# Kernel optimization log

Hardware: AMD Instinct MI355X
Metric: run time of the kernel (lower is better)

The kernel has to match this reference:

```python
import jax, jax.numpy as jnp
import numpy as np

IN_F = 1024   # in_features
OUT_F = 1024  # out_features
N = 32768     # flattened batch (prod of x.shape[:-1]))
K = 3         # clones per rewire -> denom = K + 1


def setup_inputs() -> dict:
    key = jax.random.key(0)
    k1, k2, k3, k4 = jax.random.split(key, 4)
    bound = 1.0 / np.sqrt(IN_F)
    x = jax.random.normal(k1, (N, IN_F), dtype=jnp.float32)
    # kaiming-uniform-ish init scale for weight, uniform(-bound,bound) for bias
    weight = jax.random.uniform(k2, (OUT_F, IN_F), dtype=jnp.float32,
                                minval=-bound, maxval=bound) * np.sqrt(3.0)
    bias = jax.random.uniform(k3, (OUT_F,), dtype=jnp.float32,
                              minval=-bound, maxval=bound)
    # one rewire per output row; clones are distinct from src (dead-neuron slots)
    rewire_rows = jnp.arange(OUT_F, dtype=jnp.int32)
    rewire_src = jax.random.randint(k4, (OUT_F,), 0, IN_F, dtype=jnp.int32)
    rewire_clones = (rewire_src[:, None] + jnp.arange(1, K + 1, dtype=jnp.int32)) % IN_F
    return {"x": x, "weight": weight, "bias": bias,
            "rewire_rows": rewire_rows, "rewire_src": rewire_src,
            "rewire_clones": rewire_clones}


def reference(x, weight, bias, rewire_rows, rewire_src, rewire_clones):
    # Plain linear part, shared by all output rows: y = x @ W^T + b
    base = x @ weight.T + bias                                  # [N, OUT_F]

    # Per-rewire correction. For rewire e on row r with src s and clones d_k
    # (denom = K+1), the torch loop replaces x[:, s] -> x[:, s]/denom and
    # x[:, d_k] -> x[:, s]/denom before the GEMV with weight[r].
    # Equivalent delta added to base[:, r] (indices within a rewire are disjoint):
    denom = rewire_clones.shape[1] + 1                          # K + 1
    xs = x[:, rewire_src]                                       # [N, R]
    new_val = xs / denom                                        # [N, R]
    w_src = weight[rewire_rows, rewire_src]                     # [R]
    delta = (new_val - xs) * w_src                              # src column change
    xc = x[:, rewire_clones]                                    # [N, R, K]
    wc = weight[rewire_rows[:, None], rewire_clones]            # [R, K]
    delta = delta + jnp.einsum('nrk,rk->nr', new_val[:, :, None] - xc, wc)

    # Scatter-add the deltas into their output rows (duplicates accumulate).
    return base.at[:, rewire_rows].add(delta)                   # [N, OUT_F]
```

## Files before the change

### kernel.cpp

```cpp
#include <hip/hip_runtime.h>

#define IN_F 1024
#define OUT_F 1024
#define NTOK 32768
#define BM 256
#define BN 256
#define BK 64
#define KT (IN_F / BK)

typedef __bf16 bf16;
typedef __bf16 bf16x4 __attribute__((ext_vector_type(4)));
typedef __bf16 bf16x8 __attribute__((ext_vector_type(8)));
typedef float f32x4 __attribute__((ext_vector_type(4)));

__global__ void build_wp(const float* __restrict__ W,
                         const int* __restrict__ rows,
                         const int* __restrict__ srcs,
                         const int* __restrict__ clones,
                         bf16* __restrict__ Wp) {
  const int r = blockIdx.x;
  const int row = rows[r];
  const int s = srcs[r];
  const int c0 = clones[3 * r + 0];
  const int c1 = clones[3 * r + 1];
  const int c2 = clones[3 * r + 2];
  const float* wr = W + (size_t)row * IN_F;
  const float fixv = 0.25f * (wr[s] + wr[c0] + wr[c1] + wr[c2]);

  const int col = threadIdx.x * 4;
  f32x4 v = *reinterpret_cast<const f32x4*>(wr + col);
  bf16x4 o;
#pragma unroll
  for (int j = 0; j < 4; ++j) {
    const int c = col + j;
    float f = v[j];
    if (c == c0 || c == c1 || c == c2) f = 0.0f;
    if (c == s) f = fixv;
    o[j] = (bf16)f;
  }
  *reinterpret_cast<bf16x4*>(Wp + (size_t)row * IN_F + col) = o;
}

__global__ void prep_xb(const float* __restrict__ X, bf16* __restrict__ Xb) {
  const int c = blockIdx.x * 256 + threadIdx.x;
  const int q = c & 2047;
  const int bmt = c >> 11;
  const int bm = bmt >> 4;
  const int t = bmt & 15;
  const int row = q >> 3;
  const int p = q & 7;
  const int s = p ^ (row & 7);
  const float* src = X + ((size_t)bm * BM + row) * IN_F + t * BK + s * 8;
  const f32x4 a = *reinterpret_cast<const f32x4*>(src);
  const f32x4 b = *reinterpret_cast<const f32x4*>(src + 4);
  bf16x8 o;
#pragma unroll
  for (int j = 0; j < 4; ++j) {
    o[j] = (bf16)a[j];
    o[4 + j] = (bf16)b[j];
  }
  *reinterpret_cast<bf16x8*>(Xb + (size_t)c * 8) = o;
}

__global__ __launch_bounds__(512, 2) void gemm_bf(
    const bf16* __restrict__ Xb, const bf16* __restrict__ Wp,
    const float* __restrict__ bias, float* __restrict__ out) {
  extern __shared__ __align__(16) char smem[];

  const int tid = threadIdx.x;
  const int lane = tid & 63;
  const int w = tid >> 6;
  const int wrow = w >> 2;
  const int wcol = w & 3;

  const int bid = blockIdx.x;
  const int sq = bid >> 3;
  const int bm = (bid & 7) + 8 * (sq >> 2);
  const int bn = sq & 3;

  const bf16* gA = Xb + (size_t)bm * (KT * 16384) + lane * 8;

  const bf16* gB = Wp + ((size_t)bn * BN + w * 8 + (lane >> 3)) * IN_F +
                   (((lane & 7) ^ ((lane >> 3) & 7)) * 8);

  f32x4 acc[8][4];
#pragma unroll
  for (int n = 0; n < 4; ++n) {
    const float bv = bias[bn * BN + wcol * 64 + n * 16 + (lane & 15)];
#pragma unroll
    for (int m = 0; m < 8; ++m) acc[m][n] = (f32x4){bv, bv, bv, bv};
  }

  const int rl = lane & 15;
  const int rx = rl & 7;
  const int arow0 = wrow * 128 + rl;
  const int brow0 = wcol * 64 + rl;
  const int sl0 = lane >> 4;

  auto issueA = [&](int t, int buf) {
    const bf16* g = gA + (size_t)t * 16384;
#pragma unroll
    for (int i = 0; i < 4; ++i) {
      const int chunk = i * 8 + w;
      __builtin_amdgcn_global_load_lds(
          (const __attribute__((address_space(1))) void*)(g + chunk * 512),
          (__attribute__((address_space(3))) void*)(smem + buf * 32768 +
                                                    chunk * 1024),
          16, 0, 0);
    }
  };
  auto issueB = [&](int t, int buf) {
    const bf16* g = gB + (size_t)t * BK;
    char* dst0 = smem + 65536 + buf * 32768 + w * 1024;
#pragma unroll
    for (int i = 0; i < 4; ++i) {
      __builtin_amdgcn_global_load_lds(
          (const __attribute__((address_space(1))) void*)(g +
                                                          (size_t)i * 64 * IN_F),
          (__attribute__((address_space(3))) void*)(dst0 + i * 8192), 16, 0, 0);
    }
  };
  auto compute = [&](int buf) {
    const char* A = smem + buf * 32768;
    const char* B = smem + 65536 + buf * 32768;
#pragma unroll
    for (int kk = 0; kk < 2; ++kk) {
      const int so = (((kk * 4 + sl0) ^ rx) << 4);
      bf16x8 af[8], bfr[4];
#pragma unroll
      for (int m = 0; m < 8; ++m)
        af[m] =
            *reinterpret_cast<const bf16x8*>(A + (arow0 + m * 16) * 128 + so);
#pragma unroll
      for (int n = 0; n < 4; ++n)
        bfr[n] =
            *reinterpret_cast<const bf16x8*>(B + (brow0 + n * 16) * 128 + so);
      __builtin_amdgcn_s_setprio(1);
#pragma unroll
      for (int m = 0; m < 8; ++m)
#pragma unroll
        for (int n = 0; n < 4; ++n)
          acc[m][n] = __builtin_amdgcn_mfma_f32_16x16x32_bf16(
              af[m], bfr[n], acc[m][n], 0, 0, 0);
      __builtin_amdgcn_s_setprio(0);
    }
  };

  issueA(0, 0);
  issueB(0, 0);
  __syncthreads();

  for (int t = 0; t < KT; ++t) {
    const int db = t & 1;
    if (t + 1 < KT) {
      issueA(t + 1, db ^ 1);
      issueB(t + 1, db ^ 1);
      __builtin_amdgcn_sched_barrier(0);
    }
    compute(db);
    __syncthreads();
  }

  const int orow0 = bm * BM + wrow * 128 + (lane >> 4) * 4;
  const int ocol = bn * BN + wcol * 64 + (lane & 15);
#pragma unroll
  for (int m = 0; m < 8; ++m) {
#pragma unroll
    for (int n = 0; n < 4; ++n) {
      const f32x4 v = acc[m][n];
      const size_t base = (size_t)(orow0 + m * 16) * OUT_F + (ocol + n * 16);
#pragma unroll
      for (int i = 0; i < 4; ++i) out[base + (size_t)i * OUT_F] = v[i];
    }
  }
}

__global__ __launch_bounds__(512, 2) void gemm_r4(
    const float* __restrict__ X, const bf16* __restrict__ Wp,
    const float* __restrict__ bias, float* __restrict__ out) {
  extern __shared__ __align__(16) char smem[];

  const int tid = threadIdx.x;
  const int lane = tid & 63;
  const int w = tid >> 6;
  const int wrow = w >> 2;
  const int wcol = w & 3;

  const int bid = blockIdx.x;
  const int sq = bid >> 3;
  const int bm = (bid & 7) + 8 * (sq >> 2);
  const int bn = sq & 3;

  const float* gA = X + ((size_t)bm * BM + (tid >> 3)) * IN_F + (tid & 7) * 8;
  const int awbyte =
      ((tid >> 3) << 7) + ((((tid & 7) ^ ((tid >> 3) & 7))) << 4);

  const bf16* gB = Wp + ((size_t)bn * BN + w * 8 + (lane >> 3)) * IN_F +
                   (((lane & 7) ^ ((lane >> 3) & 7)) * 8);

  f32x4 acc[8][4];
#pragma unroll
  for (int n = 0; n < 4; ++n) {
    const float bv = bias[bn * BN + wcol * 64 + n * 16 + (lane & 15)];
#pragma unroll
    for (int m = 0; m < 8; ++m) acc[m][n] = (f32x4){bv, bv, bv, bv};
  }

  const int rl = lane & 15;
  const int rx = rl & 7;
  const int arow0 = wrow * 128 + rl;
  const int brow0 = wcol * 64 + rl;
  const int sl0 = lane >> 4;

  f32x4 av[8];

  auto issueA = [&](int t) {
#pragma unroll
    for (int j = 0; j < 4; ++j) {
      const float* p = gA + (size_t)j * 64 * IN_F + (size_t)t * BK;
      av[2 * j] = *reinterpret_cast<const f32x4*>(p);
      av[2 * j + 1] = *reinterpret_cast<const f32x4*>(p + 4);
    }
  };
  auto writeA = [&](int buf) {
    char* base = smem + buf * 32768;
#pragma unroll
    for (int j = 0; j < 4; ++j) {
      bf16x8 o;
#pragma unroll
      for (int q = 0; q < 4; ++q) {
        o[q] = (bf16)av[2 * j][q];
        o[4 + q] = (bf16)av[2 * j + 1][q];
      }
      *reinterpret_cast<bf16x8*>(base + j * 8192 + awbyte) = o;
    }
  };
  auto issueB = [&](int t, int buf) {
    const bf16* g = gB + (size_t)t * BK;
    char* dst0 = smem + 65536 + buf * 32768 + w * 1024;
#pragma unroll
    for (int i = 0; i < 4; ++i) {
      __builtin_amdgcn_global_load_lds(
          (const __attribute__((address_space(1))) void*)(g +
                                                          (size_t)i * 64 * IN_F),
          (__attribute__((address_space(3))) void*)(dst0 + i * 8192), 16, 0, 0);
    }
  };
  auto compute = [&](int buf) {
    const char* A = smem + buf * 32768;
    const char* B = smem + 65536 + buf * 32768;
#pragma unroll
    for (int kk = 0; kk < 2; ++kk) {
      const int so = (((kk * 4 + sl0) ^ rx) << 4);
      bf16x8 af[8], bfr[4];
#pragma unroll
      for (int m = 0; m < 8; ++m)
        af[m] =
            *reinterpret_cast<const bf16x8*>(A + (arow0 + m * 16) * 128 + so);
#pragma unroll
      for (int n = 0; n < 4; ++n)
        bfr[n] =
            *reinterpret_cast<const bf16x8*>(B + (brow0 + n * 16) * 128 + so);
      __builtin_amdgcn_s_setprio(1);
#pragma unroll
      for (int m = 0; m < 8; ++m)
#pragma unroll
        for (int n = 0; n < 4; ++n)
          acc[m][n] = __builtin_amdgcn_mfma_f32_16x16x32_bf16(
              af[m], bfr[n], acc[m][n], 0, 0, 0);
      __builtin_amdgcn_s_setprio(0);
    }
  };

  issueA(0);
  issueB(0, 0);
  writeA(0);
  __syncthreads();

  for (int t = 0; t < KT; ++t) {
    const int db = t & 1;
    const bool more = (t + 1) < KT;
    if (more) {
      issueA(t + 1);
      issueB(t + 1, db ^ 1);
      __builtin_amdgcn_sched_barrier(0);
    }
    compute(db);
    if (more) {
      __builtin_amdgcn_sched_barrier(0);
      writeA(db ^ 1);
      __syncthreads();
    }
  }

  const int orow0 = bm * BM + wrow * 128 + (lane >> 4) * 4;
  const int ocol = bn * BN + wcol * 64 + (lane & 15);
#pragma unroll
  for (int m = 0; m < 8; ++m) {
#pragma unroll
    for (int n = 0; n < 4; ++n) {
      const f32x4 v = acc[m][n];
      const size_t base = (size_t)(orow0 + m * 16) * OUT_F + (ocol + n * 16);
#pragma unroll
      for (int i = 0; i < 4; ++i) out[base + (size_t)i * OUT_F] = v[i];
    }
  }
}

extern "C" void kernel_launch(void* const* d_in, const int* in_sizes, int n_in,
                              void* d_out, int out_size, void* d_ws,
                              size_t ws_size, hipStream_t stream) {
  const float* x = (const float*)d_in[0];
  const float* weight = (const float*)d_in[1];
  const float* bias = (const float*)d_in[2];
  const int* rrows = (const int*)d_in[3];
  const int* rsrc = (const int*)d_in[4];
  const int* rclones = (const int*)d_in[5];
  float* out = (float*)d_out;

  bf16* Wp = (bf16*)d_ws;
  bf16* Xb = (bf16*)((char*)d_ws + (2u << 20));
  const size_t need = (2u << 20) + (size_t)NTOK * IN_F * 2;

  (void)hipFuncSetAttribute((const void*)gemm_bf,
                            hipFuncAttributeMaxDynamicSharedMemorySize, 131072);
  (void)hipFuncSetAttribute((const void*)gemm_r4,
                            hipFuncAttributeMaxDynamicSharedMemorySize, 131072);

  build_wp<<<dim3(OUT_F), dim3(256), 0, stream>>>(weight, rrows, rsrc, rclones,
                                                  Wp);
  if (ws_size >= need) {
    prep_xb<<<dim3((NTOK / BM) * KT * 2048 / 256), dim3(256), 0, stream>>>(x,
                                                                           Xb);
    gemm_bf<<<dim3((NTOK / BM) * (OUT_F / BN)), dim3(512), 131072, stream>>>(
        Xb, Wp, bias, out);
  } else {
    gemm_r4<<<dim3((NTOK / BM) * (OUT_F / BN)), dim3(512), 131072, stream>>>(
        x, Wp, bias, out);
  }
}
```

Before: 116.6 us.

## Triple-buffer A tiles and prefetch two stages ahead in bf16 GEMM

The bf16 GEMM moves from a double-buffered LDS pipeline with a full __syncthreads per K-step to a three-slot ring for A tiles (two slots for B). A is prefetched two steps ahead and B one step ahead. The block barrier now waits only on partial vmcnt counts, so more global-to-LDS traffic stays in flight during MFMA compute. This raises LDS use to 160 KB and lowers launch bounds to one block per CU, giving up the second resident block in exchange for deeper prefetch. It also leans on hand-counted vmcnt values being correct.

```diff
diff --git a/kernel.cpp b/kernel.cpp
--- a/kernel.cpp
+++ b/kernel.cpp
@@ -62,7 +62,7 @@
   *reinterpret_cast<bf16x8*>(Xb + (size_t)c * 8) = o;
 }
 
-__global__ __launch_bounds__(512, 2) void gemm_bf(
+__global__ __launch_bounds__(512, 1) void gemm_bf(
     const bf16* __restrict__ Xb, const bf16* __restrict__ Wp,
     const float* __restrict__ bias, float* __restrict__ out) {
   extern __shared__ __align__(16) char smem[];
@@ -97,21 +97,21 @@
   const int brow0 = wcol * 64 + rl;
   const int sl0 = lane >> 4;
 
-  auto issueA = [&](int t, int buf) {
+  auto issueA = [&](int t, int slot) {
     const bf16* g = gA + (size_t)t * 16384;
 #pragma unroll
     for (int i = 0; i < 4; ++i) {
       const int chunk = i * 8 + w;
       __builtin_amdgcn_global_load_lds(
           (const __attribute__((address_space(1))) void*)(g + chunk * 512),
-          (__attribute__((address_space(3))) void*)(smem + buf * 32768 +
+          (__attribute__((address_space(3))) void*)(smem + slot * 32768 +
                                                     chunk * 1024),
           16, 0, 0);
     }
   };
-  auto issueB = [&](int t, int buf) {
+  auto issueB = [&](int t, int slot) {
     const bf16* g = gB + (size_t)t * BK;
-    char* dst0 = smem + 65536 + buf * 32768 + w * 1024;
+    char* dst0 = smem + 98304 + slot * 32768 + w * 1024;
 #pragma unroll
     for (int i = 0; i < 4; ++i) {
       __builtin_amdgcn_global_load_lds(
@@ -120,9 +120,9 @@
           (__attribute__((address_space(3))) void*)(dst0 + i * 8192), 16, 0, 0);
     }
   };
-  auto compute = [&](int buf) {
-    const char* A = smem + buf * 32768;
-    const char* B = smem + 65536 + buf * 32768;
+  auto compute = [&](int t) {
+    const char* A = smem + (t % 3) * 32768;
+    const char* B = smem + 98304 + (t & 1) * 32768;
 #pragma unroll
     for (int kk = 0; kk < 2; ++kk) {
       const int so = (((kk * 4 + sl0) ^ rx) << 4);
@@ -146,19 +146,26 @@
     }
   };
 
+  issueB(0, 0);
   issueA(0, 0);
-  issueB(0, 0);
-  __syncthreads();
+  issueA(1, 1);
+  asm volatile("s_waitcnt vmcnt(4)" ::: "memory");
+  __builtin_amdgcn_s_barrier();
+  __builtin_amdgcn_sched_barrier(0);
 
   for (int t = 0; t < KT; ++t) {
-    const int db = t & 1;
+    if (t + 1 < KT) issueB(t + 1, (t + 1) & 1);
+    if (t + 2 < KT) issueA(t + 2, (t + 2) % 3);
+    __builtin_amdgcn_sched_barrier(0);
+    compute(t);
     if (t + 1 < KT) {
-      issueA(t + 1, db ^ 1);
-      issueB(t + 1, db ^ 1);
+      if (t + 2 < KT)
+        asm volatile("s_waitcnt vmcnt(4)" ::: "memory");
+      else
+        asm volatile("s_waitcnt vmcnt(0)" ::: "memory");
+      __builtin_amdgcn_s_barrier();
       __builtin_amdgcn_sched_barrier(0);
     }
-    compute(db);
-    __syncthreads();
   }
 
   const int orow0 = bm * BM + wrow * 128 + (lane >> 4) * 4;
@@ -323,7 +330,7 @@
   const size_t need = (2u << 20) + (size_t)NTOK * IN_F * 2;
 
   (void)hipFuncSetAttribute((const void*)gemm_bf,
-                            hipFuncAttributeMaxDynamicSharedMemorySize, 131072);
+                            hipFuncAttributeMaxDynamicSharedMemorySize, 163840);
   (void)hipFuncSetAttribute((const void*)gemm_r4,
                             hipFuncAttributeMaxDynamicSharedMemorySize, 131072);
 
@@ -332,7 +339,7 @@
   if (ws_size >= need) {
     prep_xb<<<dim3((NTOK / BM) * KT * 2048 / 256), dim3(256), 0, stream>>>(x,
                                                                            Xb);
-    gemm_bf<<<dim3((NTOK / BM) * (OUT_F / BN)), dim3(512), 131072, stream>>>(
+    gemm_bf<<<dim3((NTOK / BM) * (OUT_F / BN)), dim3(512), 163840, stream>>>(
         Xb, Wp, bias, out);
   } else {
     gemm_r4<<<dim3((NTOK / BM) * (OUT_F / BN)), dim3(512), 131072, stream>>>(
```

Result: no change. 116.9 us (+0.3%).

## Interleave LDS reads, global prefetch and MFMA in four phases per K-tile

Applied to the files above, without the earlier changes.

Restructures the bf16 GEMM main loop into four phases per K tile. Each phase reads a slice of A fragments (B fragments are read once per tile), issues one quarter of the next tile's global-to-LDS loads, and runs 16 MFMAs. Waits and barriers are explicit (s_waitcnt and s_barrier), so memory traffic is spread across the compute instead of issued as one burst. Launch bounds are reduced to one block per SIMD group, which gives more registers but lowers occupancy. The extra barriers per tile add synchronization cost.

```diff
diff --git a/kernel.cpp b/kernel.cpp
--- a/kernel.cpp
+++ b/kernel.cpp
@@ -62,7 +62,7 @@
   *reinterpret_cast<bf16x8*>(Xb + (size_t)c * 8) = o;
 }
 
-__global__ __launch_bounds__(512, 2) void gemm_bf(
+__global__ __launch_bounds__(512, 1) void gemm_bf(
     const bf16* __restrict__ Xb, const bf16* __restrict__ Wp,
     const float* __restrict__ bias, float* __restrict__ out) {
   extern __shared__ __align__(16) char smem[];
@@ -97,68 +97,85 @@
   const int brow0 = wcol * 64 + rl;
   const int sl0 = lane >> 4;
 
-  auto issueA = [&](int t, int buf) {
+  auto gloadA1 = [&](int t, int buf, int i) {
     const bf16* g = gA + (size_t)t * 16384;
-#pragma unroll
-    for (int i = 0; i < 4; ++i) {
-      const int chunk = i * 8 + w;
-      __builtin_amdgcn_global_load_lds(
-          (const __attribute__((address_space(1))) void*)(g + chunk * 512),
-          (__attribute__((address_space(3))) void*)(smem + buf * 32768 +
-                                                    chunk * 1024),
-          16, 0, 0);
-    }
-  };
-  auto issueB = [&](int t, int buf) {
-    const bf16* g = gB + (size_t)t * BK;
-    char* dst0 = smem + 65536 + buf * 32768 + w * 1024;
-#pragma unroll
-    for (int i = 0; i < 4; ++i) {
-      __builtin_amdgcn_global_load_lds(
-          (const __attribute__((address_space(1))) void*)(g +
-                                                          (size_t)i * 64 * IN_F),
-          (__attribute__((address_space(3))) void*)(dst0 + i * 8192), 16, 0, 0);
-    }
-  };
-  auto compute = [&](int buf) {
+    const int chunk = i * 8 + w;
+    __builtin_amdgcn_global_load_lds(
+        (const __attribute__((address_space(1))) void*)(g + chunk * 512),
+        (__attribute__((address_space(3))) void*)(smem + buf * 32768 +
+                                                  chunk * 1024),
+        16, 0, 0);
+  };
+  auto gloadB1 = [&](int t, int buf, int i) {
+    const bf16* g = gB + (size_t)t * BK + (size_t)i * 64 * IN_F;
+    __builtin_amdgcn_global_load_lds(
+        (const __attribute__((address_space(1))) void*)g,
+        (__attribute__((address_space(3))) void*)(smem + 65536 + buf * 32768 +
+                                                  w * 1024 + i * 8192),
+        16, 0, 0);
+  };
+
+  bf16x8 bfr[4][2];
+  auto readB = [&](int buf) {
+    const char* B = smem + 65536 + buf * 32768;
+#pragma unroll
+    for (int n = 0; n < 4; ++n)
+#pragma unroll
+      for (int kk = 0; kk < 2; ++kk)
+        bfr[n][kk] = *reinterpret_cast<const bf16x8*>(
+            B + (brow0 + n * 16) * 128 + (((kk * 4 + sl0) ^ rx) << 4));
+  };
+  auto readA2 = [&](int buf, int m2, bf16x8 (&af)[2][2]) {
     const char* A = smem + buf * 32768;
-    const char* B = smem + 65536 + buf * 32768;
-#pragma unroll
-    for (int kk = 0; kk < 2; ++kk) {
-      const int so = (((kk * 4 + sl0) ^ rx) << 4);
-      bf16x8 af[8], bfr[4];
-#pragma unroll
-      for (int m = 0; m < 8; ++m)
-        af[m] =
-            *reinterpret_cast<const bf16x8*>(A + (arow0 + m * 16) * 128 + so);
+#pragma unroll
+    for (int dm = 0; dm < 2; ++dm)
+#pragma unroll
+      for (int kk = 0; kk < 2; ++kk)
+        af[dm][kk] = *reinterpret_cast<const bf16x8*>(
+            A + (arow0 + (m2 + dm) * 16) * 128 + (((kk * 4 + sl0) ^ rx) << 4));
+  };
+  auto mfma16 = [&](const bf16x8 (&af)[2][2], int m2) {
+    __builtin_amdgcn_s_setprio(1);
+#pragma unroll
+    for (int dm = 0; dm < 2; ++dm)
 #pragma unroll
       for (int n = 0; n < 4; ++n)
-        bfr[n] =
-            *reinterpret_cast<const bf16x8*>(B + (brow0 + n * 16) * 128 + so);
-      __builtin_amdgcn_s_setprio(1);
-#pragma unroll
-      for (int m = 0; m < 8; ++m)
-#pragma unroll
-        for (int n = 0; n < 4; ++n)
-          acc[m][n] = __builtin_amdgcn_mfma_f32_16x16x32_bf16(
-              af[m], bfr[n], acc[m][n], 0, 0, 0);
-      __builtin_amdgcn_s_setprio(0);
-    }
-  };
-
-  issueA(0, 0);
-  issueB(0, 0);
-  __syncthreads();
-
+#pragma unroll
+        for (int kk = 0; kk < 2; ++kk)
+          acc[m2 + dm][n] = __builtin_amdgcn_mfma_f32_16x16x32_bf16(
+              af[dm][kk], bfr[n][kk], acc[m2 + dm][n], 0, 0, 0);
+    __builtin_amdgcn_s_setprio(0);
+  };
+
+#pragma unroll
+  for (int i = 0; i < 4; ++i) {
+    gloadA1(0, 0, i);
+    gloadB1(0, 0, i);
+  }
+  asm volatile("s_waitcnt vmcnt(0)" ::: "memory");
+  __builtin_amdgcn_s_barrier();
+
+#pragma unroll 1
   for (int t = 0; t < KT; ++t) {
     const int db = t & 1;
-    if (t + 1 < KT) {
-      issueA(t + 1, db ^ 1);
-      issueB(t + 1, db ^ 1);
+    const int nb = db ^ 1;
+    const bool more = (t + 1) < KT;
+    bf16x8 af[2][2];
+#pragma unroll
+    for (int ph = 0; ph < 4; ++ph) {
+      if (ph == 0) readB(db);
+      readA2(db, ph * 2, af);
+      if (more) {
+        gloadA1(t + 1, nb, ph);
+        gloadB1(t + 1, nb, ph);
+      }
+      __builtin_amdgcn_s_barrier();
+      asm volatile("s_waitcnt lgkmcnt(0)" ::: "memory");
       __builtin_amdgcn_sched_barrier(0);
-    }
-    compute(db);
-    __syncthreads();
+      mfma16(af, ph * 2);
+      if (ph == 3 && more) asm volatile("s_waitcnt vmcnt(0)" ::: "memory");
+      __builtin_amdgcn_s_barrier();
+    }
   }
 
   const int orow0 = bm * BM + wrow * 128 + (lane >> 4) * 4;
```

New measurement: 121.6 us. 1.04x slower.
